# Kernel tuning notes

Hardware: AMD Instinct MI355X
Metric: run time of the kernel (lower is better)

Reference implementation:

```python
import jax, jax.numpy as jnp
import numpy as np

EPS = 1e-5
SLOPE = 0.2


def _conv(x, w, b, stride, pad):
    y = jax.lax.conv_general_dilated(
        x, w, (stride, stride), ((pad, pad), (pad, pad)),
        dimension_numbers=('NCHW', 'OIHW', 'NCHW'))
    return y + b[None, :, None, None]


def _inorm(x):
    m = x.mean(axis=(2, 3), keepdims=True)
    v = x.var(axis=(2, 3), keepdims=True)
    return (x - m) * jax.lax.rsqrt(v + EPS)


def _down(x, w, b, norm):
    y = _conv(x, w, b, 2, 1)
    if norm:
        y = _inorm(y)
    return jax.nn.leaky_relu(y, SLOPE)


def _self_attn(x, wq, bq, wk, bk, wv, bv, gamma):
    B, C, H, W = x.shape
    N = H * W
    q = _conv(x, wq, bq, 1, 0).reshape(B, -1, N)   # (B, C/8, N)
    k = _conv(x, wk, bk, 1, 0).reshape(B, -1, N)
    v = _conv(x, wv, bv, 1, 0).reshape(B, C, N)
    attn = jax.nn.softmax(jnp.einsum('bcn,bcm->bnm', q, k), axis=-1)  # (B,N,N)
    out = jnp.einsum('bcm,bnm->bcn', v, attn).reshape(B, C, H, W)
    return gamma * out + x


def _branch(p, img):
    (w0, b0, w1, b1, w2, b2, wq, bq, wk, bk, wv, bv, gamma, wh, bh) = p
    x = _down(img, w0, b0, norm=False)
    x = _down(x, w1, b1, norm=True)
    x = _self_attn(x, wq, bq, wk, bk, wv, bv, gamma)
    x = _down(x, w2, b2, norm=True)
    return _conv(x, wh, bh, 1, 1)  # head: Conv2d(nf*4, 1, 4, padding=1)


def setup_inputs() -> dict:
    key = jax.random.key(0)
    ks = jax.random.split(key, 20)
    S, B, H = 4, 16, 128
    s = 0.05  # weight scale for numerical stability of softmax energies
    d = {
        'img': jax.random.normal(ks[0], (B, 1, H, H), jnp.float32),
        'stage_idx': jax.random.randint(ks[1], (B,), 0, S, jnp.int32),
        'w0': jax.random.normal(ks[2], (S, 64, 1, 4, 4)) * s,
        'b0': jax.random.normal(ks[3], (S, 64)) * s,
        'w1': jax.random.normal(ks[4], (S, 128, 64, 4, 4)) * s,
        'b1': jax.random.normal(ks[5], (S, 128)) * s,
        'w2': jax.random.normal(ks[6], (S, 256, 128, 4, 4)) * s,
        'b2': jax.random.normal(ks[7], (S, 256)) * s,
        'wq': jax.random.normal(ks[8], (S, 16, 128, 1, 1)) * s,
        'bq': jax.random.normal(ks[9], (S, 16)) * s,
        'wk': jax.random.normal(ks[10], (S, 16, 128, 1, 1)) * s,
        'bk': jax.random.normal(ks[11], (S, 16)) * s,
        'wv': jax.random.normal(ks[12], (S, 128, 128, 1, 1)) * s,
        'bv': jax.random.normal(ks[13], (S, 128)) * s,
        'gamma': jax.random.normal(ks[14], (S,)) * s,
        'wh': jax.random.normal(ks[15], (S, 1, 256, 4, 4)) * s,
        'bh': jax.random.normal(ks[16], (S, 1)) * s,
    }
    return d


def reference(img, stage_idx, w0, b0, w1, b1, w2, b2, wq, bq, wk, bk, wv, bv, gamma, wh, bh):
    params = (w0, b0, w1, b1, w2, b2, wq, bq, wk, bk, wv, bv, gamma, wh, bh)
    # compute every branch for every sample (as the original), stacked over stage axis
    all_preds = jax.vmap(_branch, in_axes=(0, None))(params, img)  # (S, B, 1, h, w)
    B = img.shape[0]
    return all_preds[stage_idx, jnp.arange(B)]  # (B, 1, h, w)
```

## Files before the change

### kernel.cpp

```cpp
#include <hip/hip_runtime.h>

#define LRELU(x) ((x) > 0.0f ? (x) : 0.2f * (x))
#define SB __builtin_amdgcn_sched_barrier(0)

typedef short bf16x8 __attribute__((ext_vector_type(8)));
typedef short bf16x4 __attribute__((ext_vector_type(4)));
typedef float f32x4 __attribute__((ext_vector_type(4)));

__device__ __forceinline__ short f2bf(float f) {
  union { float f; unsigned u; } x{f};
  return (short)((x.u + 0x7FFF + ((x.u >> 16) & 1)) >> 16);
}

__global__ __launch_bounds__(256) void k_repack_all(
    const float* __restrict__ w1, unsigned short* __restrict__ wr1,
    const float* __restrict__ w2, unsigned short* __restrict__ wr2,
    const float* __restrict__ bh, const int* __restrict__ sidx,
    float* __restrict__ out, unsigned short* __restrict__ x0t,
    unsigned short* __restrict__ ybf, const float* __restrict__ img,
    const float* __restrict__ w0, const float* __restrict__ b0) {
  __shared__ float Ish[4 * 34];
  if (blockIdx.x >= 10517) {
    const int t = threadIdx.x;
    const int q = blockIdx.x - 10517;
    const int b = q >> 8, py = q & 255;
    const int oh = py >> 2, owb = (py & 3) << 4;
    const int s = sidx[b];
    const float* ip = img + (size_t)b * 16384;
    if (t < 136) {
      int r = t / 34, c = t % 34;
      int ih = 2 * oh - 1 + r, iw = 2 * owb - 1 + c;
      Ish[t] = ((unsigned)ih < 128u && (unsigned)iw < 128u) ? ip[ih * 128 + iw] : 0.f;
    }
    const int co = t & 63, ps = t >> 6;
    float wreg[16];
    const float* wp = w0 + (s * 64 + co) * 16;
#pragma unroll
    for (int i = 0; i < 16; i++) wreg[i] = wp[i];
    float bb = b0[s * 64 + co];
    __syncthreads();
    unsigned short* op = x0t + ((size_t)b * 4356 + (oh + 1) * 66 + (owb + 1)) * 64 + co;
#pragma unroll
    for (int j = 0; j < 4; j++) {
      int pl = ps * 4 + j;
      float acc = bb;
#pragma unroll
      for (int kh = 0; kh < 4; kh++)
#pragma unroll
        for (int kw = 0; kw < 4; kw++)
          acc += wreg[kh * 4 + kw] * Ish[kh * 34 + pl * 2 + kw];
      acc = LRELU(acc);
      op[pl * 64] = (unsigned short)f2bf(acc);
    }
    return;
  }
  int idx = blockIdx.x * 256 + threadIdx.x;
  if (idx < 524288) {
    int tap = idx & 15;
    int rest = idx >> 4;
    int ci = rest & 63, sco = rest >> 6;
    wr1[(size_t)sco * 1024 + tap * 64 + ci] = (unsigned short)f2bf(w1[idx]);
    return;
  } else if (idx < 2621440) {
    int i = idx - 524288;
    int tap = i & 15;
    int rest = i >> 4;
    int ci = rest & 127, sco = rest >> 7;
    wr2[(size_t)sco * 2048 + tap * 128 + ci] = (unsigned short)f2bf(w2[i]);
    return;
  } else if (idx < 2625040) {
    int i = idx - 2621440;
    if (i < 3600) out[i] = bh[sidx[i / 225]];
    return;
  } else if (idx < 2658320) {
    int i = idx - 2625040;
    int b = i / 2080, r = i % 2080;
    int pix = r >> 3, sub = r & 7;
    int row, col;
    if (pix < 66) { row = 0; col = pix; }
    else if (pix < 132) { row = 65; col = pix - 66; }
    else { int qq = pix - 132; row = 1 + (qq >> 1); col = (qq & 1) * 65; }
    bf16x8 z = {0, 0, 0, 0, 0, 0, 0, 0};
    *(bf16x8*)(x0t + ((size_t)b * 4356 + row * 66 + col) * 64 + sub * 8) = z;
    return;
  } else {
    int i = idx - 2658320;
    if (i >= 33792) return;
    int b = i / 2112, r = i % 2112;
    int pix = r >> 4, sub = r & 15;
    int row, col;
    if (pix < 34) { row = 0; col = pix; }
    else if (pix < 68) { row = 33; col = pix - 34; }
    else { int qq = pix - 68; row = 1 + (qq >> 1); col = (qq & 1) * 33; }
    bf16x8 z = {0, 0, 0, 0, 0, 0, 0, 0};
    *(bf16x8*)(ybf + ((size_t)b * 1156 + row * 34 + col) * 128 + sub * 8) = z;
    return;
  }
}

__global__ __launch_bounds__(256, 2) void k_conv1n(
    const unsigned short* __restrict__ x0t, const unsigned short* __restrict__ wr,
    const int* __restrict__ sidx, float* __restrict__ x1) {
  __shared__ __align__(16) unsigned short Xs[26624];
  const int t = threadIdx.x;
  const int b = blockIdx.x;
  const int y = blockIdx.y;
  const int ne = y & 15;
  const int cog = y >> 4;
  const int s = sidx[b];
  const int lane = t & 63, wv = t >> 6;
  const int quad = lane >> 4, l16 = lane & 15;

  const unsigned short* gb = x0t + ((size_t)b * 4356 + 4 * ne * 66) * 64;
  {
    float4 v[13];
#pragma unroll
    for (int i = 0; i < 13; i++) v[i] = *(const float4*)(gb + (i * 256 + t) * 8);
#pragma unroll
    for (int i = 0; i < 13; i++) {
      int ba = (i * 256 + t) * 16;
      int sw = ba ^ (((ba >> 9) & 7) << 4);
      *(float4*)((char*)Xs + sw) = v[i];
    }
  }
  __syncthreads();

  const int co0w = cog * 64 + wv * 16;
  const unsigned short* ap = wr + ((size_t)(s * 128 + co0w + l16)) * 1024 + quad * 8;
  f32x4 acc[4];
#pragma unroll
  for (int nt = 0; nt < 4; nt++) acc[nt] = (f32x4){0.f, 0.f, 0.f, 0.f};

#pragma unroll
  for (int kc = 0; kc < 32; kc++) {
    const int tap = kc >> 1;
    const int cio = (kc & 1) * 32 + quad * 8;
    const int kh = tap >> 2, kw = tap & 3;
    bf16x8 af = *(const bf16x8*)(ap + kc * 32);
#pragma unroll
    for (int nt = 0; nt < 4; nt++) {
      int lr = 2 * (nt >> 1) + kh;
      int col = 2 * ((nt & 1) * 16 + l16) + kw;
      int ba = ((lr * 66 + col) * 64 + cio) * 2;
      int sw = ba ^ (((ba >> 9) & 7) << 4);
      bf16x8 bv = *(const bf16x8*)((const char*)Xs + sw);
      acc[nt] = __builtin_amdgcn_mfma_f32_16x16x32_bf16(af, bv, acc[nt], 0, 0, 0);
    }
  }

#pragma unroll
  for (int nt = 0; nt < 4; nt++) {
    int p = ne * 64 + (nt >> 1) * 32 + (nt & 1) * 16 + l16;
#pragma unroll
    for (int r = 0; r < 4; r++)
      x1[((size_t)b * 128 + co0w + quad * 4 + r) * 1024 + p] = acc[nt][r];
  }
}

template <int NPIX>
__global__ __launch_bounds__(256) void k_inorm(float* __restrict__ x) {
  constexpr int E = NPIX / 256;
  float* p = x + (size_t)blockIdx.x * NPIX;
  const int t = threadIdx.x;
  float v[E];
  float sum = 0.f, sq = 0.f;
#pragma unroll
  for (int i = 0; i < E; i++) {
    v[i] = p[i * 256 + t];
    sum += v[i];
    sq += v[i] * v[i];
  }
#pragma unroll
  for (int o = 32; o > 0; o >>= 1) {
    sum += __shfl_down(sum, o, 64);
    sq += __shfl_down(sq, o, 64);
  }
  __shared__ float red[8];
  int wid = t >> 6;
  if ((t & 63) == 0) {
    red[wid] = sum;
    red[4 + wid] = sq;
  }
  __syncthreads();
  float S = red[0] + red[1] + red[2] + red[3];
  float SQ = red[4] + red[5] + red[6] + red[7];
  float m = S * (1.0f / NPIX);
  float var = SQ * (1.0f / NPIX) - m * m;
  float inv = rsqrtf(var + 1e-5f);
#pragma unroll
  for (int i = 0; i < E; i++) p[i * 256 + t] = LRELU((v[i] - m) * inv);
}

template <int NPIX>
__global__ __launch_bounds__(256) void k_inormw(float* __restrict__ x) {
  constexpr int E = NPIX / 256;
  const int wv = threadIdx.x >> 6, lane = threadIdx.x & 63;
  const size_t row = (size_t)blockIdx.x * 4 + wv;
  float4* p = (float4*)(x + row * NPIX);
  float4 v[E];
#pragma unroll
  for (int i = 0; i < E; i++) v[i] = p[i * 64 + lane];
  float sum = 0.f, sq = 0.f;
#pragma unroll
  for (int i = 0; i < E; i++) {
    sum += v[i].x + v[i].y + v[i].z + v[i].w;
    sq += v[i].x * v[i].x + v[i].y * v[i].y + v[i].z * v[i].z + v[i].w * v[i].w;
  }
#pragma unroll
  for (int o = 32; o > 0; o >>= 1) {
    sum += __shfl_xor(sum, o, 64);
    sq += __shfl_xor(sq, o, 64);
  }
  float m = sum * (1.0f / NPIX);
  float var = sq * (1.0f / NPIX) - m * m;
  float inv = rsqrtf(var + 1e-5f);
#pragma unroll
  for (int i = 0; i < E; i++) {
    v[i].x = LRELU((v[i].x - m) * inv);
    v[i].y = LRELU((v[i].y - m) * inv);
    v[i].z = LRELU((v[i].z - m) * inv);
    v[i].w = LRELU((v[i].w - m) * inv);
    p[i * 64 + lane] = v[i];
  }
}

__global__ __launch_bounds__(256) void k_proj_qkv(
    const float* __restrict__ xin, const float* __restrict__ wq,
    const float* __restrict__ bq, const float* __restrict__ wk,
    const float* __restrict__ bk, const float* __restrict__ wv,
    const float* __restrict__ bv, const int* __restrict__ sidx,
    float* __restrict__ q, float* __restrict__ kout, unsigned short* __restrict__ vpk) {
  __shared__ float xsh[32 * 256];
  __shared__ float wsh[16 * 32];
  const int t = threadIdx.x;
  const int b = blockIdx.x;
  const int y = blockIdx.y;
  const int s = sidx[b];
  const int cg = t >> 6, ng = t & 63;
  const float* w;
  const float* bias;
  int co0, nn0, CO;
  if (y < 8) {
    w = (y < 4) ? wq : wk;
    bias = (y < 4) ? bq : bk;
    co0 = 0;
    nn0 = (y & 3) * 256;
    CO = 16;
  } else {
    w = wv;
    bias = bv;
    co0 = ((y - 8) >> 2) * 16;
    nn0 = ((y - 8) & 3) * 256;
    CO = 128;
  }
  const float* xb = xin + (size_t)b * 128 * 1024;
  float4 acc4[4];
#pragma unroll
  for (int c = 0; c < 4; c++) {
    float bb = bias[s * CO + co0 + cg * 4 + c];
    acc4[c] = make_float4(bb, bb, bb, bb);
  }
  for (int cc = 0; cc < 4; cc++) {
#pragma unroll
    for (int k = 0; k < 8; k++) {
      int id = t + (k << 8);
      int ci = id >> 6, nf = id & 63;
      ((float4*)xsh)[id] = ((const float4*)(xb + (cc * 32 + ci) * 1024 + nn0))[nf];
    }
    if (t < 128)
      ((float4*)wsh)[t] =
          ((const float4*)(w + ((size_t)(s * CO + co0 + (t >> 3))) * 128 + cc * 32))[t & 7];
    __syncthreads();
#pragma unroll
    for (int ci4 = 0; ci4 < 8; ci4++) {
      float4 wvv[4], xv[4];
#pragma unroll
      for (int c = 0; c < 4; c++) wvv[c] = ((const float4*)wsh)[(cg * 4 + c) * 8 + ci4];
#pragma unroll
      for (int i = 0; i < 4; i++) xv[i] = ((const float4*)xsh)[(ci4 * 4 + i) * 64 + ng];
#pragma unroll
      for (int c = 0; c < 4; c++)
#pragma unroll
        for (int i = 0; i < 4; i++) {
          float wvc = i == 0 ? wvv[c].x : i == 1 ? wvv[c].y : i == 2 ? wvv[c].z : wvv[c].w;
          acc4[c].x += wvc * xv[i].x;
          acc4[c].y += wvc * xv[i].y;
          acc4[c].z += wvc * xv[i].z;
          acc4[c].w += wvc * xv[i].w;
        }
    }
    __syncthreads();
  }
  if (y < 8) {
    float* out = (y < 4) ? q : kout;
#pragma unroll
    for (int c = 0; c < 4; c++)
      ((float4*)(out + ((size_t)b * 16 + cg * 4 + c) * 1024 + nn0))[ng] = acc4[c];
  } else {
    int n = nn0 + ng * 4;
#pragma unroll
    for (int c = 0; c < 4; c++) {
      int co = co0 + cg * 4 + c;
      bf16x4 u;
      u[0] = f2bf(acc4[c].x);
      u[1] = f2bf(acc4[c].y);
      u[2] = f2bf(acc4[c].z);
      u[3] = f2bf(acc4[c].w);
      *(bf16x4*)(vpk + (((size_t)b * 32 + (n >> 5)) * 128 + co) * 32 + (n & 31)) = u;
    }
  }
}

__global__ __launch_bounds__(256, 2) void k_attn(
    const float* __restrict__ q, const float* __restrict__ k,
    const unsigned short* __restrict__ vpk, const float* __restrict__ x1,
    const float* __restrict__ gamma, const int* __restrict__ sidx,
    unsigned short* __restrict__ ybf) {
  __shared__ __align__(16) short Psh[16 * 1032];
  __shared__ float qsh[256];
  __shared__ float redm[64], reds[64];
  const int t = threadIdx.x;
  const int b = blockIdx.x >> 6;
  const int n0 = (blockIdx.x & 63) << 4;
  const int lane = t & 63, wv = t >> 6;
  const int quad = lane >> 4, l16 = lane & 15;
  const float* qb = q + (size_t)b * 16 * 1024;
  const float* kb = k + (size_t)b * 16 * 1024;
  const float* xb = x1 + (size_t)b * 128 * 1024;

  qsh[t] = qb[((t >> 4) << 10) + n0 + (t & 15)];
  __syncthreads();

  float acc[4][16];
#pragma unroll
  for (int j = 0; j < 4; j++)
#pragma unroll
    for (int nl = 0; nl < 16; nl++) acc[j][nl] = 0.0f;

  float4 KA[4], KB[4];
#define LDK(BUF, G)                                                       \
  _Pragma("unroll") for (int c4 = 0; c4 < 4; c4++)                        \
      BUF[c4] = *(const float4*)(kb + ((((G) * 4 + c4)) << 10) + 4 * t);  \
  SB;
#define MMK(BUF, G)                                                                         \
  _Pragma("unroll") for (int c4 = 0; c4 < 4; c4++) {                                        \
    const float* qr = qsh + ((G) * 4 + c4) * 16;                                            \
    _Pragma("unroll") for (int j = 0; j < 4; j++) {                                         \
      float kk = j == 0 ? BUF[c4].x : j == 1 ? BUF[c4].y : j == 2 ? BUF[c4].z : BUF[c4].w;  \
      _Pragma("unroll") for (int nl = 0; nl < 16; nl++) acc[j][nl] += kk * qr[nl];          \
    }                                                                                       \
  }                                                                                         \
  SB;

  LDK(KA, 0)
  LDK(KB, 1)
  MMK(KA, 0) LDK(KA, 2)
  MMK(KB, 1) LDK(KB, 3)
  MMK(KA, 2)
  MMK(KB, 3)
#undef LDK
#undef MMK

  float lmax[16];
#pragma unroll
  for (int nl = 0; nl < 16; nl++)
    lmax[nl] = fmaxf(fmaxf(acc[0][nl], acc[1][nl]), fmaxf(acc[2][nl], acc[3][nl]));
#pragma unroll
  for (int o = 32; o > 0; o >>= 1)
#pragma unroll
    for (int nl = 0; nl < 16; nl++) lmax[nl] = fmaxf(lmax[nl], __shfl_xor(lmax[nl], o, 64));
  if (lane == 0)
#pragma unroll
    for (int nl = 0; nl < 16; nl++) redm[wv * 16 + nl] = lmax[nl];
  __syncthreads();
#pragma unroll
  for (int nl = 0; nl < 16; nl++)
    lmax[nl] = fmaxf(fmaxf(redm[nl], redm[16 + nl]), fmaxf(redm[32 + nl], redm[48 + nl]));
  float lsum[16];
#pragma unroll
  for (int nl = 0; nl < 16; nl++) lsum[nl] = 0.0f;
#pragma unroll
  for (int j = 0; j < 4; j++)
#pragma unroll
    for (int nl = 0; nl < 16; nl++) {
      float e = __expf(acc[j][nl] - lmax[nl]);
      acc[j][nl] = e;
      lsum[nl] += e;
    }
#pragma unroll
  for (int o = 32; o > 0; o >>= 1)
#pragma unroll
    for (int nl = 0; nl < 16; nl++) lsum[nl] += __shfl_xor(lsum[nl], o, 64);
  if (lane == 0)
#pragma unroll
    for (int nl = 0; nl < 16; nl++) reds[wv * 16 + nl] = lsum[nl];
#pragma unroll
  for (int nl = 0; nl < 16; nl++) {
    bf16x4 pv;
    pv[0] = f2bf(acc[0][nl]);
    pv[1] = f2bf(acc[1][nl]);
    pv[2] = f2bf(acc[2][nl]);
    pv[3] = f2bf(acc[3][nl]);
    *(bf16x4*)&Psh[nl * 1032 + 4 * t] = pv;
  }
  __syncthreads();

  const unsigned short* vp =
      vpk + ((size_t)b * 32 * 128 + (size_t)(wv * 32 + l16)) * 32 + quad * 8;
  const short* prow = Psh + l16 * 1032 + quad * 8;
  f32x4 dacc[2];
  dacc[0] = (f32x4){0.f, 0.f, 0.f, 0.f};
  dacc[1] = (f32x4){0.f, 0.f, 0.f, 0.f};

  bf16x8 VA0[4], VA1[4], PAr[4];
  bf16x8 VB0[4], VB1[4], PBr[4];
#define LDV(V0, V1, PR, G)                                \
  _Pragma("unroll") for (int m4 = 0; m4 < 4; m4++) {      \
    int mt = (G) * 4 + m4;                                \
    V0[m4] = *(const bf16x8*)(vp + mt * 4096);            \
    V1[m4] = *(const bf16x8*)(vp + 512 + mt * 4096);      \
    PR[m4] = *(const bf16x8*)(prow + mt * 32);            \
  }                                                       \
  SB;
#define MMV(V0, V1, PR)                                                                      \
  _Pragma("unroll") for (int m4 = 0; m4 < 4; m4++) {                                         \
    dacc[0] = __builtin_amdgcn_mfma_f32_16x16x32_bf16(V0[m4], PR[m4], dacc[0], 0, 0, 0);     \
    dacc[1] = __builtin_amdgcn_mfma_f32_16x16x32_bf16(V1[m4], PR[m4], dacc[1], 0, 0, 0);     \
  }                                                                                          \
  SB;

  LDV(VA0, VA1, PAr, 0)
  LDV(VB0, VB1, PBr, 1)
  MMV(VA0, VA1, PAr) LDV(VA0, VA1, PAr, 2)
  MMV(VB0, VB1, PBr) LDV(VB0, VB1, PBr, 3)
  MMV(VA0, VA1, PAr) LDV(VA0, VA1, PAr, 4)
  MMV(VB0, VB1, PBr) LDV(VB0, VB1, PBr, 5)
  MMV(VA0, VA1, PAr) LDV(VA0, VA1, PAr, 6)
  MMV(VB0, VB1, PBr) LDV(VB0, VB1, PBr, 7)
  MMV(VA0, VA1, PAr)
  MMV(VB0, VB1, PBr)
#undef LDV
#undef MMV
  __syncthreads();

  float* Osh = (float*)Psh;
  short* Osh2 = Psh + 4352;
#pragma unroll
  for (int i = 0; i < 2; i++) {
    int cob = wv * 32 + i * 16 + quad * 4;
#pragma unroll
    for (int r = 0; r < 4; r++) Osh[(cob + r) * 17 + l16] = dacc[i][r];
  }
  __syncthreads();
  float g = gamma[sidx[b]];
  {
    int co = t >> 1, j0 = (t & 1) * 8;
    const float* xr = xb + (co << 10) + n0 + j0;
    float4 xv0 = *(const float4*)xr;
    float4 xv1 = *(const float4*)(xr + 4);
    float xs[8] = {xv0.x, xv0.y, xv0.z, xv0.w, xv1.x, xv1.y, xv1.z, xv1.w};
#pragma unroll
    for (int j = 0; j < 8; j++) {
      int nl = j0 + j;
      float rs = 1.0f / (reds[nl] + reds[16 + nl] + reds[32 + nl] + reds[48 + nl]);
      Osh2[nl * 136 + co] = f2bf(g * Osh[co * 17 + nl] * rs + xs[j]);
    }
  }
  __syncthreads();
  {
    int nl = t >> 4, cg = t & 15;
    bf16x8 u = *(const bf16x8*)&Osh2[nl * 136 + cg * 8];
    int p = n0 + nl;
    int ih = p >> 5, iw = p & 31;
    *(bf16x8*)(ybf + ((size_t)b * 1156 + (ih + 1) * 34 + (iw + 1)) * 128 + cg * 8) = u;
  }
}

__global__ __launch_bounds__(256, 2) void k_conv2n(
    const unsigned short* __restrict__ ybf, const unsigned short* __restrict__ wr,
    const int* __restrict__ sidx, float* __restrict__ x2) {
  __shared__ __align__(16) unsigned short Xs[26624];
  const int t = threadIdx.x;
  const int b = blockIdx.x;
  const int y = blockIdx.y;
  const int ne = y & 7;
  const int cog = y >> 3;
  const int s = sidx[b];
  const int lane = t & 63, wv = t >> 6;
  const int quad = lane >> 4, l16 = lane & 15;

  const unsigned short* gb = ybf + ((size_t)b * 1156 + 4 * ne * 34) * 128;
  {
    float4 v[13];
#pragma unroll
    for (int i = 0; i < 13; i++) v[i] = *(const float4*)(gb + (i * 256 + t) * 8);
#pragma unroll
    for (int i = 0; i < 13; i++) {
      int ba = (i * 256 + t) * 16;
      int sw = ba ^ (((ba >> 9) & 7) << 4);
      *(float4*)((char*)Xs + sw) = v[i];
    }
  }
  __syncthreads();

  const int co0w = cog * 64 + wv * 16;
  const unsigned short* ap = wr + ((size_t)(s * 256 + co0w + l16)) * 2048 + quad * 8;
  f32x4 acc[2];
  acc[0] = (f32x4){0.f, 0.f, 0.f, 0.f};
  acc[1] = (f32x4){0.f, 0.f, 0.f, 0.f};

#pragma unroll
  for (int kc = 0; kc < 64; kc++) {
    const int tap = kc >> 2;
    const int cio = (kc & 3) * 32 + quad * 8;
    const int kh = tap >> 2, kw = tap & 3;
    bf16x8 af = *(const bf16x8*)(ap + kc * 32);
#pragma unroll
    for (int nt = 0; nt < 2; nt++) {
      int lr = 2 * nt + kh;
      int col = 2 * l16 + kw;
      int ba = ((lr * 34 + col) * 128 + cio) * 2;
      int sw = ba ^ (((ba >> 9) & 7) << 4);
      bf16x8 bv = *(const bf16x8*)((const char*)Xs + sw);
      acc[nt] = __builtin_amdgcn_mfma_f32_16x16x32_bf16(af, bv, acc[nt], 0, 0, 0);
    }
  }

#pragma unroll
  for (int nt = 0; nt < 2; nt++) {
    int p = ne * 32 + nt * 16 + l16;
#pragma unroll
    for (int r = 0; r < 4; r++)
      x2[((size_t)b * 256 + co0w + quad * 4 + r) * 256 + p] = acc[nt][r];
  }
}

__global__ __launch_bounds__(256) void k_head_part(
    const float* __restrict__ x2, const float* __restrict__ wh,
    const int* __restrict__ sidx, float* __restrict__ out) {
  __shared__ float Xs[32 * 256];
  __shared__ float Wsh[512];
  const int t = threadIdx.x;
  const int b = blockIdx.x, cc = blockIdx.y;
  const int s = sidx[b];
  const float* xp = x2 + ((size_t)b * 256 + cc * 32) * 256;
#pragma unroll
  for (int i = 0; i < 32; i++) Xs[i * 256 + t] = xp[i * 256 + t];
#pragma unroll
  for (int i = 0; i < 2; i++) {
    int idx = i * 256 + t;
    Wsh[idx] = wh[s * 4096 + cc * 512 + idx];
  }
  __syncthreads();
  if (t < 225) {
    int oh = t / 15, ow = t % 15;
    float acc = 0.0f;
    for (int ci = 0; ci < 32; ci++) {
      const float* xr = Xs + ci * 256;
      const float* wr = Wsh + ci * 16;
#pragma unroll
      for (int kh = 0; kh < 4; kh++) {
        int ih = oh - 1 + kh;
        if ((unsigned)ih >= 16u) continue;
#pragma unroll
        for (int kw = 0; kw < 4; kw++) {
          int iw = ow - 1 + kw;
          if ((unsigned)iw >= 16u) continue;
          acc += wr[kh * 4 + kw] * xr[(ih << 4) + iw];
        }
      }
    }
    atomicAdd(out + b * 225 + t, acc);
  }
}

extern "C" void kernel_launch(void* const* d_in, const int* in_sizes, int n_in,
                              void* d_out, int out_size, void* d_ws, size_t ws_size,
                              hipStream_t stream) {
  const float* img = (const float*)d_in[0];
  const int* sidx = (const int*)d_in[1];
  const float* w0 = (const float*)d_in[2];
  const float* b0 = (const float*)d_in[3];
  const float* w1 = (const float*)d_in[4];
  const float* w2 = (const float*)d_in[6];
  const float* wq = (const float*)d_in[8];
  const float* bq = (const float*)d_in[9];
  const float* wk = (const float*)d_in[10];
  const float* bk = (const float*)d_in[11];
  const float* wv = (const float*)d_in[12];
  const float* bv = (const float*)d_in[13];
  const float* gamma = (const float*)d_in[14];
  const float* wh = (const float*)d_in[15];
  const float* bh = (const float*)d_in[16];
  float* out = (float*)d_out;

  float* ws = (float*)d_ws;
  unsigned short* x0t = (unsigned short*)(ws);
  float* x1 = ws + 2359296;
  float* q = ws + 4456448;
  float* k = ws + 4718592;
  unsigned short* vpk = (unsigned short*)(ws + 4980736);
  unsigned short* ybf = (unsigned short*)(ws + 6029312);
  float* x2 = ws + 7340032;
  unsigned short* wr1 = (unsigned short*)(ws + 8912896);
  unsigned short* wr2 = (unsigned short*)(ws + 9175040);

  const int B = 16;

  k_repack_all<<<14613, 256, 0, stream>>>(w1, wr1, w2, wr2, bh, sidx, out, x0t, ybf,
                                          img, w0, b0);
  k_conv1n<<<dim3(B, 32), 256, 0, stream>>>(x0t, wr1, sidx, x1);
  k_inorm<1024><<<B * 128, 256, 0, stream>>>(x1);
  k_proj_qkv<<<dim3(B, 40), 256, 0, stream>>>(x1, wq, bq, wk, bk, wv, bv, sidx, q, k, vpk);
  k_attn<<<B * 64, 256, 0, stream>>>(q, k, vpk, x1, gamma, sidx, ybf);
  k_conv2n<<<dim3(B, 32), 256, 0, stream>>>(ybf, wr2, sidx, x2);
  k_inormw<256><<<1024, 256, 0, stream>>>(x2);
  k_head_part<<<dim3(B, 8), 256, 0, stream>>>(x2, wh, sidx, out);
}
```

Baseline: 206.5 us.

## Fuse final instance norm into head conv and vectorize weight repack

Removes the separate k_inormw launch: the head kernel now computes per-channel mean/variance on the 32x256 tile it already holds in shared memory, then normalizes and applies leaky ReLU before the head convolution. The weight repack now has each thread read a float4 (four taps), so the repack needs far fewer blocks. This saves one launch and a global read/write pass over x2, at the cost of extra reduction work and syncs inside the head kernel.

```diff
diff --git a/kernel.cpp b/kernel.cpp
--- a/kernel.cpp
+++ b/kernel.cpp
@@ -20,9 +20,9 @@
     unsigned short* __restrict__ ybf, const float* __restrict__ img,
     const float* __restrict__ w0, const float* __restrict__ b0) {
   __shared__ float Ish[4 * 34];
-  if (blockIdx.x >= 10517) {
+  if (blockIdx.x >= 2837) {
     const int t = threadIdx.x;
-    const int q = blockIdx.x - 10517;
+    const int q = blockIdx.x - 2837;
     const int b = q >> 8, py = q & 255;
     const int oh = py >> 2, owb = (py & 3) << 4;
     const int s = sidx[b];
@@ -55,25 +55,37 @@
     return;
   }
   int idx = blockIdx.x * 256 + threadIdx.x;
-  if (idx < 524288) {
-    int tap = idx & 15;
-    int rest = idx >> 4;
+  if (idx < 131072) {
+    float4 v = *(const float4*)(w1 + (size_t)idx * 4);
+    int base = idx * 4;
+    int tap0 = base & 15;
+    int rest = base >> 4;
     int ci = rest & 63, sco = rest >> 6;
-    wr1[(size_t)sco * 1024 + tap * 64 + ci] = (unsigned short)f2bf(w1[idx]);
+    unsigned short* d = wr1 + (size_t)sco * 1024 + ci;
+    d[(tap0 + 0) * 64] = (unsigned short)f2bf(v.x);
+    d[(tap0 + 1) * 64] = (unsigned short)f2bf(v.y);
+    d[(tap0 + 2) * 64] = (unsigned short)f2bf(v.z);
+    d[(tap0 + 3) * 64] = (unsigned short)f2bf(v.w);
     return;
-  } else if (idx < 2621440) {
-    int i = idx - 524288;
-    int tap = i & 15;
-    int rest = i >> 4;
+  } else if (idx < 655360) {
+    int i = idx - 131072;
+    float4 v = *(const float4*)(w2 + (size_t)i * 4);
+    int base = i * 4;
+    int tap0 = base & 15;
+    int rest = base >> 4;
     int ci = rest & 127, sco = rest >> 7;
-    wr2[(size_t)sco * 2048 + tap * 128 + ci] = (unsigned short)f2bf(w2[i]);
+    unsigned short* d = wr2 + (size_t)sco * 2048 + ci;
+    d[(tap0 + 0) * 128] = (unsigned short)f2bf(v.x);
+    d[(tap0 + 1) * 128] = (unsigned short)f2bf(v.y);
+    d[(tap0 + 2) * 128] = (unsigned short)f2bf(v.z);
+    d[(tap0 + 3) * 128] = (unsigned short)f2bf(v.w);
     return;
-  } else if (idx < 2625040) {
-    int i = idx - 2621440;
+  } else if (idx < 658960) {
+    int i = idx - 655360;
     if (i < 3600) out[i] = bh[sidx[i / 225]];
     return;
-  } else if (idx < 2658320) {
-    int i = idx - 2625040;
+  } else if (idx < 692240) {
+    int i = idx - 658960;
     int b = i / 2080, r = i % 2080;
     int pix = r >> 3, sub = r & 7;
     int row, col;
@@ -84,7 +96,7 @@
     *(bf16x8*)(x0t + ((size_t)b * 4356 + row * 66 + col) * 64 + sub * 8) = z;
     return;
   } else {
-    int i = idx - 2658320;
+    int i = idx - 692240;
     if (i >= 33792) return;
     int b = i / 2112, r = i % 2112;
     int pix = r >> 4, sub = r & 15;
@@ -189,39 +201,6 @@
   float inv = rsqrtf(var + 1e-5f);
 #pragma unroll
   for (int i = 0; i < E; i++) p[i * 256 + t] = LRELU((v[i] - m) * inv);
-}
-
-template <int NPIX>
-__global__ __launch_bounds__(256) void k_inormw(float* __restrict__ x) {
-  constexpr int E = NPIX / 256;
-  const int wv = threadIdx.x >> 6, lane = threadIdx.x & 63;
-  const size_t row = (size_t)blockIdx.x * 4 + wv;
-  float4* p = (float4*)(x + row * NPIX);
-  float4 v[E];
-#pragma unroll
-  for (int i = 0; i < E; i++) v[i] = p[i * 64 + lane];
-  float sum = 0.f, sq = 0.f;
-#pragma unroll
-  for (int i = 0; i < E; i++) {
-    sum += v[i].x + v[i].y + v[i].z + v[i].w;
-    sq += v[i].x * v[i].x + v[i].y * v[i].y + v[i].z * v[i].z + v[i].w * v[i].w;
-  }
-#pragma unroll
-  for (int o = 32; o > 0; o >>= 1) {
-    sum += __shfl_xor(sum, o, 64);
-    sq += __shfl_xor(sq, o, 64);
-  }
-  float m = sum * (1.0f / NPIX);
-  float var = sq * (1.0f / NPIX) - m * m;
-  float inv = rsqrtf(var + 1e-5f);
-#pragma unroll
-  for (int i = 0; i < E; i++) {
-    v[i].x = LRELU((v[i].x - m) * inv);
-    v[i].y = LRELU((v[i].y - m) * inv);
-    v[i].z = LRELU((v[i].z - m) * inv);
-    v[i].w = LRELU((v[i].w - m) * inv);
-    p[i * 64 + lane] = v[i];
-  }
 }
 
 __global__ __launch_bounds__(256) void k_proj_qkv(
@@ -540,6 +519,7 @@
     const int* __restrict__ sidx, float* __restrict__ out) {
   __shared__ float Xs[32 * 256];
   __shared__ float Wsh[512];
+  __shared__ float sm[32], si[32];
   const int t = threadIdx.x;
   const int b = blockIdx.x, cc = blockIdx.y;
   const int s = sidx[b];
@@ -550,6 +530,34 @@
   for (int i = 0; i < 2; i++) {
     int idx = i * 256 + t;
     Wsh[idx] = wh[s * 4096 + cc * 512 + idx];
+  }
+  __syncthreads();
+  {
+    int r = t >> 3, c0 = (t & 7) * 32;
+    float sv = 0.f, sq = 0.f;
+#pragma unroll
+    for (int j = 0; j < 32; j++) {
+      float v = Xs[r * 256 + c0 + j];
+      sv += v;
+      sq += v * v;
+    }
+#pragma unroll
+    for (int o = 1; o < 8; o <<= 1) {
+      sv += __shfl_xor(sv, o, 64);
+      sq += __shfl_xor(sq, o, 64);
+    }
+    if ((t & 7) == 0) {
+      float m = sv * (1.0f / 256.0f);
+      float var = sq * (1.0f / 256.0f) - m * m;
+      sm[r] = m;
+      si[r] = rsqrtf(var + 1e-5f);
+    }
+  }
+  __syncthreads();
+#pragma unroll
+  for (int i = 0; i < 32; i++) {
+    float v = (Xs[i * 256 + t] - sm[i]) * si[i];
+    Xs[i * 256 + t] = LRELU(v);
   }
   __syncthreads();
   if (t < 225) {
@@ -607,13 +615,12 @@
 
   const int B = 16;
 
-  k_repack_all<<<14613, 256, 0, stream>>>(w1, wr1, w2, wr2, bh, sidx, out, x0t, ybf,
-                                          img, w0, b0);
+  k_repack_all<<<6933, 256, 0, stream>>>(w1, wr1, w2, wr2, bh, sidx, out, x0t, ybf,
+                                         img, w0, b0);
   k_conv1n<<<dim3(B, 32), 256, 0, stream>>>(x0t, wr1, sidx, x1);
   k_inorm<1024><<<B * 128, 256, 0, stream>>>(x1);
   k_proj_qkv<<<dim3(B, 40), 256, 0, stream>>>(x1, wq, bq, wk, bk, wv, bv, sidx, q, k, vpk);
   k_attn<<<B * 64, 256, 0, stream>>>(q, k, vpk, x1, gamma, sidx, ybf);
   k_conv2n<<<dim3(B, 32), 256, 0, stream>>>(ybf, wr2, sidx, x2);
-  k_inormw<256><<<1024, 256, 0, stream>>>(x2);
   k_head_part<<<dim3(B, 8), 256, 0, stream>>>(x2, wh, sidx, out);
 }
```

Measured after the change: 201.0 us. -2.6%, faster.
